# Performance work log

Hardware: AMD Instinct MI355X
Metric: run time of the kernel (lower is better)

The kernel has to match this reference:

```python
import jax, jax.numpy as jnp
import numpy as np

EPS = 1e-08


def setup_inputs() -> dict:
    key = jax.random.key(0)
    k_x, k_w1, k_b1, k_w2, k_b2 = jax.random.split(key, 5)
    B, C, T = 64, 64, 4000
    x = jax.random.normal(k_x, (B, C, T, 1), dtype=jnp.float32)
    # 1x1 Conv2D with in_channels=1, out_channels=8 -> weight is an 8-vector + bias
    w1 = jax.random.normal(k_w1, (8,), dtype=jnp.float32) * 0.5
    b1 = jax.random.normal(k_b1, (8,), dtype=jnp.float32) * 0.1
    w2 = jax.random.normal(k_w2, (8,), dtype=jnp.float32) * 0.5
    b2 = jax.random.normal(k_b2, (8,), dtype=jnp.float32) * 0.1
    # gamma is initialized to 0 in the module (residual identity at init);
    # use a nonzero value so the attention path is exercised numerically.
    gamma = jnp.float32(0.5)
    return {"x": x, "w1": w1, "b1": b1, "w2": w2, "b2": b2, "gamma": gamma}


def reference(x, w1, b1, w2, b2, gamma):
    B, C, T, _ = x.shape  # (B, num_ch, T, 1)
    # 1x1 conv with C_in=1: broadcast multiply-add, then flatten (T, 8) -> T*8
    q = (x * w1 + b1).reshape(B, C, T * 8)  # proj_query (B, C, T*8)
    k = (x * w2 + b2).reshape(B, C, T * 8)  # proj_key   (B, C, T*8)
    # energy = Q @ K^T  -> (B, C, C)
    energy = jnp.einsum('bcd,bed->bce', q, k)
    # custom min-max normalization along last axis, then softmax
    max_h = jnp.max(energy, axis=2, keepdims=True)
    min_h = jnp.min(energy, axis=2, keepdims=True)
    energy = (energy - min_h) / (max_h - min_h + EPS)
    attention = jax.nn.softmax(energy, axis=-1)
    xs = x[..., 0]  # squeeze last dim -> (B, C, T)
    # attention^T @ xs  (transpose_a=True)
    attended = jnp.einsum('bec,bet->bct', attention, xs)
    return gamma * attended[..., None] + x
```

## Files before the change

kernel.cpp:

```cpp
#include <hip/hip_runtime.h>

#define BB 64
#define CC 64
#define TT 4000

#define SLABS 8
#define TSLAB 250
#define SLABT (2 * TSLAB)
#define GP_PITCH 264

#define TPB 128
#define NT2 ((TT + TPB - 1) / TPB)
#define XPITCH 132
#define APITCH 72

#define GPART_ELEMS ((size_t)SLABS * BB * CC * CC)
#define SPART_ELEMS ((size_t)SLABS * BB * CC)

typedef short short8 __attribute__((ext_vector_type(8)));
typedef float f32x16 __attribute__((ext_vector_type(16)));

__device__ __forceinline__ short f2bf(float f) {
    unsigned u = __float_as_uint(f);
    u = (u + 0x7FFFu + ((u >> 16) & 1u)) >> 16;
    return (short)u;
}
__device__ __forceinline__ float bfpair(unsigned u) {
    return __uint_as_float(u << 16) + __uint_as_float(u & 0xFFFF0000u);
}

__global__ __launch_bounds__(256)
void gram_mfma(const float* __restrict__ x, float* __restrict__ G_part,
               float* __restrict__ S_part) {
    __shared__ short xs[CC * GP_PITCH];
    __shared__ float sred[4 * 64];
    const int b    = blockIdx.x / SLABS;
    const int slab = blockIdx.x % SLABS;
    const int tid  = threadIdx.x;
    const int lane = tid & 63;
    const int wave = tid >> 6;
    const float* xb = x + (size_t)b * CC * TT;

    const int r0 = (wave >> 1) * 32, c0 = (wave & 1) * 32;
    const int m = lane & 31, half = lane >> 5;
    f32x16 acc;
    #pragma unroll
    for (int z = 0; z < 16; ++z) acc[z] = 0.f;
    float s_acc = 0.f;

    for (int ch = 0; ch < 2; ++ch) {
        const int t0 = slab * SLABT + ch * TSLAB;

        #pragma unroll
        for (int g = 0; g < 2; ++g) {
            float4 v[8];
            #pragma unroll
            for (int k = 0; k < 8; ++k) {
                const int i = tid + 256 * (g * 8 + k);
                const int row = i >> 6, tq = i & 63;
                float4 w = make_float4(0.f, 0.f, 0.f, 0.f);
                if (tq < 62) {
                    w = *(const float4*)(xb + row * TT + t0 + 4 * tq);
                } else if (tq == 62) {
                    const float* p = xb + row * TT + t0 + 248;
                    w.x = p[0]; w.y = p[1];
                }
                v[k] = w;
            }
            #pragma unroll
            for (int k = 0; k < 8; ++k) {
                const int i = tid + 256 * (g * 8 + k);
                const int row = i >> 6, tq = i & 63;
                short4 sv;
                sv.x = f2bf(v[k].x); sv.y = f2bf(v[k].y);
                sv.z = f2bf(v[k].z); sv.w = f2bf(v[k].w);
                const int pc = (tq >> 1) ^ (row & 7);
                *(short4*)(xs + row * GP_PITCH + pc * 8 + (tq & 1) * 4) = sv;
            }
        }
        __syncthreads();

        {
            const short* rowp = xs + lane * GP_PITCH;
            #pragma unroll
            for (int j = 0; j < 8; ++j) {
                const int pc = (wave * 8 + j) ^ (lane & 7);
                uint2 u0 = *(const uint2*)(rowp + pc * 8);
                uint2 u1 = *(const uint2*)(rowp + pc * 8 + 4);
                s_acc += bfpair(u0.x) + bfpair(u0.y) + bfpair(u1.x) + bfpair(u1.y);
            }
        }

        #pragma unroll
        for (int ks = 0; ks < 16; ++ks) {
            const int ck = ks * 2 + half;
            short8 av = *(const short8*)(xs + (r0 + m) * GP_PITCH + (ck ^ (m & 7)) * 8);
            short8 bv = *(const short8*)(xs + (c0 + m) * GP_PITCH + (ck ^ (m & 7)) * 8);
            acc = __builtin_amdgcn_mfma_f32_32x32x16_bf16(av, bv, acc, 0, 0, 0);
        }
        __syncthreads();
    }

    sred[wave * 64 + lane] = s_acc;
    __syncthreads();
    if (tid < 64) {
        float s = sred[tid] + sred[64 + tid] + sred[128 + tid] + sred[192 + tid];
        S_part[(slab * BB + b) * CC + tid] = s;
    }

    float* gp = G_part + ((size_t)slab * BB + b) * (CC * CC);
    #pragma unroll
    for (int r = 0; r < 16; ++r) {
        const int row = (r & 3) + 8 * (r >> 2) + 4 * half;
        gp[(r0 + row) * CC + (c0 + m)] = acc[r];
    }
}

__global__ __launch_bounds__(256)
void softmax_fused(const float* __restrict__ w1, const float* __restrict__ b1,
                   const float* __restrict__ w2, const float* __restrict__ b2,
                   const float* __restrict__ G_part, const float* __restrict__ S_part,
                   unsigned short* __restrict__ attB) {
    __shared__ float Es[64 * 65];
    __shared__ float Sb[64];
    __shared__ float red_mn[4 * 64], red_mx[4 * 64], red_sm[4 * 64];
    const int b   = blockIdx.x;
    const int tid = threadIdx.x;
    const int c = tid & 63, q = tid >> 6;

    #pragma unroll
    for (int j4 = 0; j4 < 4; ++j4) {
        const int jj = tid + 256 * j4;
        float4 s = make_float4(0.f, 0.f, 0.f, 0.f);
        #pragma unroll
        for (int sl = 0; sl < SLABS; ++sl) {
            const float4 g = *(const float4*)(G_part + ((size_t)sl * BB + b) * 4096 + 4 * jj);
            s.x += g.x; s.y += g.y; s.z += g.z; s.w += g.w;
        }
        const int row = jj >> 4, col = (jj & 15) * 4;
        float* e = Es + row * 65 + col;
        e[0] = s.x; e[1] = s.y; e[2] = s.z; e[3] = s.w;
    }
    if (tid < 64) {
        float s = 0.f;
        #pragma unroll
        for (int sl = 0; sl < SLABS; ++sl)
            s += S_part[(sl * BB + b) * CC + tid];
        Sb[tid] = s;
    }
    float A = 0.f, Bc = 0.f, Be = 0.f, Cc = 0.f;
    #pragma unroll
    for (int j = 0; j < 8; ++j) {
        float a1 = w1[j], a2 = w2[j], q1 = b1[j], q2 = b2[j];
        A += a1 * a2; Bc += a1 * q2; Be += q1 * a2; Cc += q1 * q2;
    }
    Cc *= (float)TT;
    __syncthreads();

    const float sc = Sb[c];
    float ev[16], mn = 1e30f, mx = -1e30f;
    #pragma unroll
    for (int i = 0; i < 16; ++i) {
        const int e = 16 * q + i;
        float en = A * Es[c * 65 + e] + Bc * sc + Be * Sb[e] + Cc;
        ev[i] = en;
        mn = fminf(mn, en); mx = fmaxf(mx, en);
    }
    red_mn[q * 64 + c] = mn; red_mx[q * 64 + c] = mx;
    __syncthreads();
    mn = fminf(fminf(red_mn[c], red_mn[64 + c]), fminf(red_mn[128 + c], red_mn[192 + c]));
    mx = fmaxf(fmaxf(red_mx[c], red_mx[64 + c]), fmaxf(red_mx[128 + c], red_mx[192 + c]));
    const float ninv = 1.f / (mx - mn + 1e-8f);
    float pv[16], ls = 0.f;
    #pragma unroll
    for (int i = 0; i < 16; ++i) {
        float p = __expf((ev[i] - mn) * ninv);
        pv[i] = p; ls += p;
    }
    red_sm[q * 64 + c] = ls;
    __syncthreads();
    const float rinv = 1.f / (red_sm[c] + red_sm[64 + c] + red_sm[128 + c] + red_sm[192 + c]);
    #pragma unroll
    for (int i = 0; i < 16; ++i) Es[c * 65 + 16 * q + i] = pv[i] * rinv;
    __syncthreads();
    unsigned short* ab = attB + (size_t)b * 4096;
    #pragma unroll
    for (int j2 = tid; j2 < 2048; j2 += 256) {
        const int cc = j2 >> 5, e0 = (j2 & 31) * 2;
        const unsigned lo = (unsigned short)f2bf(Es[e0 * 65 + cc]);
        const unsigned hi = (unsigned short)f2bf(Es[(e0 + 1) * 65 + cc]);
        *(unsigned*)(ab + cc * 64 + e0) = lo | (hi << 16);
    }
}

__global__ __launch_bounds__(256)
void apply_mfma(const float* __restrict__ x, const unsigned short* __restrict__ attB,
                const float* __restrict__ gamma, float* __restrict__ out) {
    __shared__ float xs[CC * XPITCH];
    __shared__ short al[CC * APITCH];
    const int b  = blockIdx.x / NT2;
    const int t0 = (blockIdx.x % NT2) * TPB;
    const int tid = threadIdx.x;
    const int lane = tid & 63, wave = tid >> 6;
    const float* xb = x + (size_t)b * CC * TT;
    const unsigned short* ab = attB + (size_t)b * 4096;

    short8 avv[2];
    #pragma unroll
    for (int k = 0; k < 2; ++k)
        avv[k] = *(const short8*)(ab + (tid + 256 * k) * 8);

    #pragma unroll
    for (int g = 0; g < 2; ++g) {
        float4 v[4];
        #pragma unroll
        for (int k = 0; k < 4; ++k) {
            const int i = tid + 256 * (g * 4 + k);
            const int e = i >> 5, p = i & 31;
            const int t = t0 + 4 * p;
            v[k] = make_float4(0.f, 0.f, 0.f, 0.f);
            if (t < TT) v[k] = *(const float4*)(xb + e * TT + t);
        }
        #pragma unroll
        for (int k = 0; k < 4; ++k) {
            const int i = tid + 256 * (g * 4 + k);
            const int e = i >> 5, p = i & 31;
            *(float4*)(xs + e * XPITCH + 4 * p) = v[k];
        }
    }
    #pragma unroll
    for (int k = 0; k < 2; ++k) {
        const int i = tid + 256 * k;
        const int cch = i >> 3, q8 = i & 7;
        *(short8*)(al + cch * APITCH + q8 * 8) = avv[k];
    }
    __syncthreads();

    const int m = lane & 31, half = lane >> 5;
    const int c0 = (wave & 1) * 32;
    const int tb = (wave >> 1) * 64;
    f32x16 acc0, acc1;
    #pragma unroll
    for (int z = 0; z < 16; ++z) { acc0[z] = 0.f; acc1[z] = 0.f; }

    #pragma unroll
    for (int ks = 0; ks < 4; ++ks) {
        short8 av = *(const short8*)(al + (c0 + m) * APITCH + ks * 16 + 8 * half);
        const int eb = ks * 16 + 8 * half;
        short8 bv0, bv1;
        #pragma unroll
        for (int j = 0; j < 8; ++j) {
            bv0[j] = f2bf(xs[(eb + j) * XPITCH + tb + m]);
            bv1[j] = f2bf(xs[(eb + j) * XPITCH + tb + 32 + m]);
        }
        acc0 = __builtin_amdgcn_mfma_f32_32x32x16_bf16(av, bv0, acc0, 0, 0, 0);
        acc1 = __builtin_amdgcn_mfma_f32_32x32x16_bf16(av, bv1, acc1, 0, 0, 0);
    }

    const float gm = gamma[0];
    float* ob = out + (size_t)b * CC * TT;
    #pragma unroll
    for (int r = 0; r < 16; ++r) {
        const int row = (r & 3) + 8 * (r >> 2) + 4 * half;
        const int c = c0 + row;
        const int tl0 = tb + m, tl1 = tb + 32 + m;
        const int tg0 = t0 + tl0, tg1 = t0 + tl1;
        if (tg0 < TT) ob[c * TT + tg0] = gm * acc0[r] + xs[c * XPITCH + tl0];
        if (tg1 < TT) ob[c * TT + tg1] = gm * acc1[r] + xs[c * XPITCH + tl1];
    }
}

extern "C" void kernel_launch(void* const* d_in, const int* in_sizes, int n_in,
                              void* d_out, int out_size, void* d_ws, size_t ws_size,
                              hipStream_t stream) {
    const float* x  = (const float*)d_in[0];
    const float* w1 = (const float*)d_in[1];
    const float* b1 = (const float*)d_in[2];
    const float* w2 = (const float*)d_in[3];
    const float* b2 = (const float*)d_in[4];
    const float* gm = (const float*)d_in[5];
    float* out = (float*)d_out;

    float* G_part = (float*)d_ws;
    float* S_part = G_part + GPART_ELEMS;
    unsigned short* attB = (unsigned short*)(S_part + SPART_ELEMS);

    hipLaunchKernelGGL(gram_mfma, dim3(BB * SLABS), dim3(256), 0, stream,
                       x, G_part, S_part);
    hipLaunchKernelGGL(softmax_fused, dim3(BB), dim3(256), 0, stream,
                       w1, b1, w2, b2, G_part, S_part, attB);
    hipLaunchKernelGGL(apply_mfma, dim3(BB * NT2), dim3(256), 0, stream,
                       x, attB, gm, out);
}
```

Baseline: 156.3 us.

## Fuse softmax into apply kernel, recomputing attention per time slab

Merges the separate softmax and apply kernels into one kernel launched over batch × slab blocks. Each block recomputes the 64x64 attention softmax from the partial Gram sums and writes it straight to shared memory as bf16, then loops over four 128-step time tiles within its 500-step slab. This drops one kernel launch and the global round-trip of the attention matrix. In exchange the softmax work is repeated eight times per batch, grid parallelism falls from 64×32 to 512 blocks, and the tile loads in the time loop are serialized with no overlap.

```diff
diff --git a/kernel.cpp b/kernel.cpp
--- a/kernel.cpp
+++ b/kernel.cpp
@@ -10,12 +10,10 @@
 #define GP_PITCH 264
 
 #define TPB 128
-#define NT2 ((TT + TPB - 1) / TPB)
 #define XPITCH 132
 #define APITCH 72
 
 #define GPART_ELEMS ((size_t)SLABS * BB * CC * CC)
-#define SPART_ELEMS ((size_t)SLABS * BB * CC)
 
 typedef short short8 __attribute__((ext_vector_type(8)));
 typedef float f32x16 __attribute__((ext_vector_type(16)));
@@ -117,156 +115,142 @@
 }
 
 __global__ __launch_bounds__(256)
-void softmax_fused(const float* __restrict__ w1, const float* __restrict__ b1,
+void softmax_apply(const float* __restrict__ x,
+                   const float* __restrict__ w1, const float* __restrict__ b1,
                    const float* __restrict__ w2, const float* __restrict__ b2,
                    const float* __restrict__ G_part, const float* __restrict__ S_part,
-                   unsigned short* __restrict__ attB) {
-    __shared__ float Es[64 * 65];
+                   const float* __restrict__ gamma, float* __restrict__ out) {
+    __shared__ float xsbuf[CC * XPITCH];
+    __shared__ short al[CC * APITCH];
+    __shared__ float red[3 * 256];
     __shared__ float Sb[64];
-    __shared__ float red_mn[4 * 64], red_mx[4 * 64], red_sm[4 * 64];
-    const int b   = blockIdx.x;
-    const int tid = threadIdx.x;
-    const int c = tid & 63, q = tid >> 6;
-
-    #pragma unroll
-    for (int j4 = 0; j4 < 4; ++j4) {
-        const int jj = tid + 256 * j4;
-        float4 s = make_float4(0.f, 0.f, 0.f, 0.f);
-        #pragma unroll
-        for (int sl = 0; sl < SLABS; ++sl) {
-            const float4 g = *(const float4*)(G_part + ((size_t)sl * BB + b) * 4096 + 4 * jj);
-            s.x += g.x; s.y += g.y; s.z += g.z; s.w += g.w;
-        }
-        const int row = jj >> 4, col = (jj & 15) * 4;
-        float* e = Es + row * 65 + col;
-        e[0] = s.x; e[1] = s.y; e[2] = s.z; e[3] = s.w;
-    }
-    if (tid < 64) {
-        float s = 0.f;
-        #pragma unroll
-        for (int sl = 0; sl < SLABS; ++sl)
-            s += S_part[(sl * BB + b) * CC + tid];
-        Sb[tid] = s;
-    }
-    float A = 0.f, Bc = 0.f, Be = 0.f, Cc = 0.f;
-    #pragma unroll
-    for (int j = 0; j < 8; ++j) {
-        float a1 = w1[j], a2 = w2[j], q1 = b1[j], q2 = b2[j];
-        A += a1 * a2; Bc += a1 * q2; Be += q1 * a2; Cc += q1 * q2;
-    }
-    Cc *= (float)TT;
-    __syncthreads();
-
-    const float sc = Sb[c];
-    float ev[16], mn = 1e30f, mx = -1e30f;
-    #pragma unroll
-    for (int i = 0; i < 16; ++i) {
-        const int e = 16 * q + i;
-        float en = A * Es[c * 65 + e] + Bc * sc + Be * Sb[e] + Cc;
-        ev[i] = en;
-        mn = fminf(mn, en); mx = fmaxf(mx, en);
-    }
-    red_mn[q * 64 + c] = mn; red_mx[q * 64 + c] = mx;
-    __syncthreads();
-    mn = fminf(fminf(red_mn[c], red_mn[64 + c]), fminf(red_mn[128 + c], red_mn[192 + c]));
-    mx = fmaxf(fmaxf(red_mx[c], red_mx[64 + c]), fmaxf(red_mx[128 + c], red_mx[192 + c]));
-    const float ninv = 1.f / (mx - mn + 1e-8f);
-    float pv[16], ls = 0.f;
-    #pragma unroll
-    for (int i = 0; i < 16; ++i) {
-        float p = __expf((ev[i] - mn) * ninv);
-        pv[i] = p; ls += p;
-    }
-    red_sm[q * 64 + c] = ls;
-    __syncthreads();
-    const float rinv = 1.f / (red_sm[c] + red_sm[64 + c] + red_sm[128 + c] + red_sm[192 + c]);
-    #pragma unroll
-    for (int i = 0; i < 16; ++i) Es[c * 65 + 16 * q + i] = pv[i] * rinv;
-    __syncthreads();
-    unsigned short* ab = attB + (size_t)b * 4096;
-    #pragma unroll
-    for (int j2 = tid; j2 < 2048; j2 += 256) {
-        const int cc = j2 >> 5, e0 = (j2 & 31) * 2;
-        const unsigned lo = (unsigned short)f2bf(Es[e0 * 65 + cc]);
-        const unsigned hi = (unsigned short)f2bf(Es[(e0 + 1) * 65 + cc]);
-        *(unsigned*)(ab + cc * 64 + e0) = lo | (hi << 16);
-    }
-}
-
-__global__ __launch_bounds__(256)
-void apply_mfma(const float* __restrict__ x, const unsigned short* __restrict__ attB,
-                const float* __restrict__ gamma, float* __restrict__ out) {
-    __shared__ float xs[CC * XPITCH];
-    __shared__ short al[CC * APITCH];
-    const int b  = blockIdx.x / NT2;
-    const int t0 = (blockIdx.x % NT2) * TPB;
-    const int tid = threadIdx.x;
+    const int tid  = threadIdx.x;
     const int lane = tid & 63, wave = tid >> 6;
+    const int b    = blockIdx.x & 63;
+    const int slab = blockIdx.x >> 6;
     const float* xb = x + (size_t)b * CC * TT;
-    const unsigned short* ab = attB + (size_t)b * 4096;
-
-    short8 avv[2];
-    #pragma unroll
-    for (int k = 0; k < 2; ++k)
-        avv[k] = *(const short8*)(ab + (tid + 256 * k) * 8);
-
-    #pragma unroll
-    for (int g = 0; g < 2; ++g) {
-        float4 v[4];
-        #pragma unroll
-        for (int k = 0; k < 4; ++k) {
-            const int i = tid + 256 * (g * 4 + k);
-            const int e = i >> 5, p = i & 31;
-            const int t = t0 + 4 * p;
-            v[k] = make_float4(0.f, 0.f, 0.f, 0.f);
-            if (t < TT) v[k] = *(const float4*)(xb + e * TT + t);
-        }
-        #pragma unroll
-        for (int k = 0; k < 4; ++k) {
-            const int i = tid + 256 * (g * 4 + k);
-            const int e = i >> 5, p = i & 31;
-            *(float4*)(xs + e * XPITCH + 4 * p) = v[k];
-        }
-    }
-    #pragma unroll
-    for (int k = 0; k < 2; ++k) {
-        const int i = tid + 256 * k;
-        const int cch = i >> 3, q8 = i & 7;
-        *(short8*)(al + cch * APITCH + q8 * 8) = avv[k];
-    }
-    __syncthreads();
-
     const int m = lane & 31, half = lane >> 5;
-    const int c0 = (wave & 1) * 32;
-    const int tb = (wave >> 1) * 64;
-    f32x16 acc0, acc1;
-    #pragma unroll
-    for (int z = 0; z < 16; ++z) { acc0[z] = 0.f; acc1[z] = 0.f; }
-
-    #pragma unroll
-    for (int ks = 0; ks < 4; ++ks) {
-        short8 av = *(const short8*)(al + (c0 + m) * APITCH + ks * 16 + 8 * half);
-        const int eb = ks * 16 + 8 * half;
-        short8 bv0, bv1;
+
+    {
+        float* Es = xsbuf;
+        #pragma unroll
+        for (int j4 = 0; j4 < 4; ++j4) {
+            const int jj = tid + 256 * j4;
+            float4 s = make_float4(0.f, 0.f, 0.f, 0.f);
+            #pragma unroll
+            for (int sl = 0; sl < SLABS; ++sl) {
+                const float4 g = *(const float4*)(G_part + ((size_t)sl * BB + b) * 4096 + 4 * jj);
+                s.x += g.x; s.y += g.y; s.z += g.z; s.w += g.w;
+            }
+            const int row = jj >> 4, col = (jj & 15) * 4;
+            float* e = Es + row * 65 + col;
+            e[0] = s.x; e[1] = s.y; e[2] = s.z; e[3] = s.w;
+        }
+        if (tid < 64) {
+            float s = 0.f;
+            #pragma unroll
+            for (int sl = 0; sl < SLABS; ++sl)
+                s += S_part[(sl * BB + b) * CC + tid];
+            Sb[tid] = s;
+        }
+        float A = 0.f, Bc = 0.f, Be = 0.f, Cc = 0.f;
         #pragma unroll
         for (int j = 0; j < 8; ++j) {
-            bv0[j] = f2bf(xs[(eb + j) * XPITCH + tb + m]);
-            bv1[j] = f2bf(xs[(eb + j) * XPITCH + tb + 32 + m]);
-        }
-        acc0 = __builtin_amdgcn_mfma_f32_32x32x16_bf16(av, bv0, acc0, 0, 0, 0);
-        acc1 = __builtin_amdgcn_mfma_f32_32x32x16_bf16(av, bv1, acc1, 0, 0, 0);
-    }
-
-    const float gm = gamma[0];
-    float* ob = out + (size_t)b * CC * TT;
-    #pragma unroll
-    for (int r = 0; r < 16; ++r) {
-        const int row = (r & 3) + 8 * (r >> 2) + 4 * half;
-        const int c = c0 + row;
-        const int tl0 = tb + m, tl1 = tb + 32 + m;
-        const int tg0 = t0 + tl0, tg1 = t0 + tl1;
-        if (tg0 < TT) ob[c * TT + tg0] = gm * acc0[r] + xs[c * XPITCH + tl0];
-        if (tg1 < TT) ob[c * TT + tg1] = gm * acc1[r] + xs[c * XPITCH + tl1];
+            float a1 = w1[j], a2 = w2[j], q1 = b1[j], q2 = b2[j];
+            A += a1 * a2; Bc += a1 * q2; Be += q1 * a2; Cc += q1 * q2;
+        }
+        Cc *= (float)TT;
+        __syncthreads();
+
+        const int c = tid & 63, q = tid >> 6;
+        const float sc = Sb[c];
+        float ev[16], mn = 1e30f, mx = -1e30f;
+        #pragma unroll
+        for (int i = 0; i < 16; ++i) {
+            const int e = 16 * q + i;
+            float en = A * Es[c * 65 + e] + Bc * sc + Be * Sb[e] + Cc;
+            ev[i] = en;
+            mn = fminf(mn, en); mx = fmaxf(mx, en);
+        }
+        red[q * 64 + c] = mn; red[256 + q * 64 + c] = mx;
+        __syncthreads();
+        mn = fminf(fminf(red[c], red[64 + c]), fminf(red[128 + c], red[192 + c]));
+        mx = fmaxf(fmaxf(red[256 + c], red[320 + c]), fmaxf(red[384 + c], red[448 + c]));
+        const float ninv = 1.f / (mx - mn + 1e-8f);
+        float pv[16], ls = 0.f;
+        #pragma unroll
+        for (int i = 0; i < 16; ++i) {
+            float p = __expf((ev[i] - mn) * ninv);
+            pv[i] = p; ls += p;
+        }
+        red[512 + q * 64 + c] = ls;
+        __syncthreads();
+        const float rinv = 1.f / (red[512 + c] + red[576 + c] + red[640 + c] + red[704 + c]);
+        #pragma unroll
+        for (int i = 0; i < 16; ++i)
+            al[(16 * q + i) * APITCH + c] = f2bf(pv[i] * rinv);
+        __syncthreads();
+    }
+
+    {
+        const int c0 = (wave & 1) * 32;
+        const int tb = (wave >> 1) * 64;
+        const float gm = gamma[0];
+        float* ob = out + (size_t)b * CC * TT;
+        const int t0s = slab * SLABT;
+
+        for (int it = 0; it < 4; ++it) {
+            const int t0l = it * TPB;
+            const int t0  = t0s + t0l;
+            #pragma unroll
+            for (int g2 = 0; g2 < 2; ++g2) {
+                float4 v[4];
+                #pragma unroll
+                for (int k = 0; k < 4; ++k) {
+                    const int i = tid + 256 * (g2 * 4 + k);
+                    const int e = i >> 5, p = i & 31;
+                    const int t = t0 + 4 * p;
+                    v[k] = make_float4(0.f, 0.f, 0.f, 0.f);
+                    if (t < TT) v[k] = *(const float4*)(xb + e * TT + t);
+                }
+                #pragma unroll
+                for (int k = 0; k < 4; ++k) {
+                    const int i = tid + 256 * (g2 * 4 + k);
+                    const int e = i >> 5, p = i & 31;
+                    *(float4*)(xsbuf + e * XPITCH + 4 * p) = v[k];
+                }
+            }
+            __syncthreads();
+
+            f32x16 acc0, acc1;
+            #pragma unroll
+            for (int z = 0; z < 16; ++z) { acc0[z] = 0.f; acc1[z] = 0.f; }
+            #pragma unroll
+            for (int ks = 0; ks < 4; ++ks) {
+                short8 av = *(const short8*)(al + (c0 + m) * APITCH + ks * 16 + 8 * half);
+                const int eb = ks * 16 + 8 * half;
+                short8 bv0, bv1;
+                #pragma unroll
+                for (int j = 0; j < 8; ++j) {
+                    bv0[j] = f2bf(xsbuf[(eb + j) * XPITCH + tb + m]);
+                    bv1[j] = f2bf(xsbuf[(eb + j) * XPITCH + tb + 32 + m]);
+                }
+                acc0 = __builtin_amdgcn_mfma_f32_32x32x16_bf16(av, bv0, acc0, 0, 0, 0);
+                acc1 = __builtin_amdgcn_mfma_f32_32x32x16_bf16(av, bv1, acc1, 0, 0, 0);
+            }
+
+            #pragma unroll
+            for (int r = 0; r < 16; ++r) {
+                const int row = (r & 3) + 8 * (r >> 2) + 4 * half;
+                const int c = c0 + row;
+                const int tl0 = tb + m, tl1 = tb + 32 + m;
+                if (t0l + tl0 < SLABT)
+                    ob[c * TT + t0 + tl0] = gm * acc0[r] + xsbuf[c * XPITCH + tl0];
+                if (t0l + tl1 < SLABT)
+                    ob[c * TT + t0 + tl1] = gm * acc1[r] + xsbuf[c * XPITCH + tl1];
+            }
+            __syncthreads();
+        }
     }
 }
 
@@ -283,12 +267,9 @@
 
     float* G_part = (float*)d_ws;
     float* S_part = G_part + GPART_ELEMS;
-    unsigned short* attB = (unsigned short*)(S_part + SPART_ELEMS);
 
     hipLaunchKernelGGL(gram_mfma, dim3(BB * SLABS), dim3(256), 0, stream,
                        x, G_part, S_part);
-    hipLaunchKernelGGL(softmax_fused, dim3(BB), dim3(256), 0, stream,
-                       w1, b1, w2, b2, G_part, S_part, attB);
-    hipLaunchKernelGGL(apply_mfma, dim3(BB * NT2), dim3(256), 0, stream,
-                       x, attB, gm, out);
-}
+    hipLaunchKernelGGL(softmax_apply, dim3(BB * SLABS), dim3(256), 0, stream,
+                       x, w1, b1, w2, b2, G_part, S_part, gm, out);
+}
```

Measured after the change: 157.4 us. About the same (+0.6%).
